# Optimization experiments

Measured on AMD Instinct MI355X. Metric: run time of the kernel, lower is better.

## Reference

```python
import jax, jax.numpy as jnp
import numpy as np

T, B, D, H = 512, 256, 256, 512


def setup_inputs() -> dict:
    key = jax.random.key(0)
    k1, k2, k3, k4 = jax.random.split(key, 4)
    x = jax.random.normal(k1, (T, B, D), dtype=jnp.float32)
    hidden_state = jnp.zeros((1, B, H), dtype=jnp.float32)
    episode_starts = jax.random.randint(k2, (T, B), 0, 2, dtype=jnp.int32)
    # PyTorch GRU params, gate order (r, z, n); xavier-ish / orthogonal-ish scale via randn*scale
    w_ih = jax.random.normal(k3, (3 * H, D), dtype=jnp.float32) * (1.0 / np.sqrt(D))
    w_hh = jax.random.normal(k4, (3 * H, H), dtype=jnp.float32) * (1.0 / np.sqrt(H))
    b_ih = jnp.zeros((3 * H,), dtype=jnp.float32)
    b_hh = jnp.zeros((3 * H,), dtype=jnp.float32)
    return {"x": x, "hidden_state": hidden_state, "episode_starts": episode_starts,
            "w_ih": w_ih, "w_hh": w_hh, "b_ih": b_ih, "b_hh": b_hh}


def _gru_scan(x, h0, episode_starts, w_ih, w_hh, b_ih, b_hh):
    # Precompute input projections for all timesteps: [T, B, 3H]
    gi_all = jnp.einsum('tbd,gd->tbg', x, w_ih) + b_ih
    keep_all = 1.0 - (episode_starts != 0).astype(x.dtype)  # [T, B]
    hsz = h0.shape[-1]

    def step(h, inputs):
        gi, keep = inputs          # gi: [B, 3H], keep: [B]
        h = h * keep[:, None]      # episode reset
        gh = h @ w_hh.T + b_hh     # [B, 3H]
        gi_r, gi_z, gi_n = gi[:, :hsz], gi[:, hsz:2 * hsz], gi[:, 2 * hsz:]
        gh_r, gh_z, gh_n = gh[:, :hsz], gh[:, hsz:2 * hsz], gh[:, 2 * hsz:]
        r = jax.nn.sigmoid(gi_r + gh_r)
        z = jax.nn.sigmoid(gi_z + gh_z)
        n = jnp.tanh(gi_n + r * gh_n)
        h_new = (1.0 - z) * n + z * h
        return h_new, h_new

    h_final, outputs = jax.lax.scan(step, h0, (gi_all, keep_all))
    return outputs, h_final


def reference(x, hidden_state, episode_starts, w_ih, w_hh, b_ih, b_hh):
    h0 = hidden_state[0]  # num_layers=1 -> [B, H]
    outputs, h_final = _gru_scan(x, h0, episode_starts, w_ih, w_hh, b_ih, b_hh)
    return outputs, h_final[None]  # ([T, B, H], [1, B, H])
```

## Files before the change

### kernel.cpp

```cpp
#include <hip/hip_runtime.h>
#include <stdint.h>

#define TT 512
#define BB 256
#define DD 256
#define HH 512

#define WSL 32
#define NGROUP 16
#define KS_X 8
#define KS_H 16
#define KS_TOT 24
#define NBLK 144

typedef __attribute__((ext_vector_type(8))) short short8;
typedef __attribute__((ext_vector_type(4))) float floatx4;
typedef __attribute__((ext_vector_type(4))) unsigned int uintx4;

__device__ __forceinline__ short f2bf(float v) {
    union { float f; uint32_t u; } x; x.f = v;
    uint32_t r = (x.u + 0x7fffu + ((x.u >> 16) & 1u)) >> 16;
    return (short)r;
}
__device__ __forceinline__ float bf2f_hi(unsigned int s) {
    union { uint32_t u; float f; } x; x.u = s & 0xffff0000u;
    return x.f;
}
__device__ __forceinline__ float sigm(float v) { return 1.0f / (1.0f + __expf(-v)); }

__global__ __launch_bounds__(256)
void clear_exch(unsigned int* e) {
    uintx4 v = {0xFFFFFFFFu, 0xFFFFFFFFu, 0xFFFFFFFFu, 0xFFFFFFFFu};
    *(uintx4*)(e + ((size_t)blockIdx.x * 256 + threadIdx.x) * 4) = v;
}

__global__ __launch_bounds__(128, 1)
void gru_persistent(const float* __restrict__ x,
                    const float* __restrict__ h0,
                    const int*   __restrict__ ep,
                    const float* __restrict__ w_ih,
                    const float* __restrict__ w_hh,
                    const float* __restrict__ b_ih,
                    const float* __restrict__ b_hh,
                    float* __restrict__ out,
                    unsigned int* __restrict__ exch) {
    __shared__ short ldsw[NBLK * 512];

    const int tid  = threadIdx.x;
    const int lane = tid & 63;
    const int w    = tid >> 6;
    const int b    = blockIdx.x;
    const int xcd = b & 7;
    const int idx = b >> 3;
    const int bg  = xcd * 2 + (idx >> 4);
    const int sl  = idx & 15;

    for (int u = tid; u < NBLK * 64; u += 128) {
        int blk = u >> 6;
        int l   = u & 63;
        int ww  = blk / 72;
        int rem = blk % 72;
        int g   = rem / 24;
        int ks  = rem % 24;
        int row = sl * WSL + ww * 16 + (l & 15) + g * HH;
        int k0  = ks * 32 + ((l >> 4) * 8);
        const float* src = (k0 < DD) ? (w_ih + (size_t)row * DD + k0)
                                     : (w_hh + (size_t)row * HH + (k0 - DD));
        short8 v;
        #pragma unroll
        for (int j = 0; j < 8; j++) v[j] = f2bf(src[j]);
        *(short8*)&ldsw[(size_t)blk * 512 + l * 8] = v;
    }
    __syncthreads();

    const int cl   = lane & 15;
    const int col  = sl * WSL + w * 16 + cl;
    const int am   = bg * 16 + cl;
    const int rbase = (lane >> 4) * 4;
    const int k0a  = (lane >> 4) * 8;
    const float br0 = b_ih[col] + b_hh[col];
    const float bz0 = b_ih[col + HH] + b_hh[col + HH];
    const float bin = b_ih[col + 2 * HH];
    const float bhn = b_hh[col + 2 * HH];

    for (int t = 0; t < TT; t++) {
        floatx4 accI[3], accH[3];
        #pragma unroll
        for (int g = 0; g < 3; g++) {
            accI[g] = (floatx4){0.f, 0.f, 0.f, 0.f};
            accH[g] = (floatx4){0.f, 0.f, 0.f, 0.f};
        }

        const float* xrow = x + ((size_t)t * BB + am) * DD;
        #pragma unroll
        for (int ks = 0; ks < KS_X; ks++) {
            int k0 = ks * 32 + k0a;
            short8 a;
            #pragma unroll
            for (int j = 0; j < 8; j++) a[j] = f2bf(xrow[k0 + j]);
            #pragma unroll
            for (int g = 0; g < 3; g++) {
                short8 bf = *(const short8*)&ldsw[(size_t)((w * 3 + g) * KS_TOT + ks) * 512 + lane * 8];
                accI[g] = __builtin_amdgcn_mfma_f32_16x16x32_bf16(a, bf, accI[g], 0, 0, 0);
            }
        }
        const float keepA = (ep[t * BB + am] != 0) ? 0.0f : 1.0f;

        short8 a[KS_H];
        float hprev_raw[4];
        if (t == 0) {
            const float* hrow = h0 + (size_t)am * HH;
            #pragma unroll
            for (int ks = 0; ks < KS_H; ks++) {
                int k0 = ks * 32 + k0a;
                #pragma unroll
                for (int j = 0; j < 8; j++) a[ks][j] = f2bf(hrow[k0 + j] * keepA);
            }
            #pragma unroll
            for (int j = 0; j < 4; j++)
                hprev_raw[j] = h0[(size_t)(bg * 16 + rbase + j) * HH + col];
        } else {
            const unsigned int tgt = (unsigned int)(t - 1);
            const unsigned int* exr = exch + ((size_t)((t & 1) ^ 1)) * BB * HH;
            const unsigned int* hb  = exr + (size_t)am * HH + k0a;
            const unsigned int* hq0 = exr + (size_t)(bg * 16 + rbase) * HH + col;
            const unsigned int* hq2 = exr + (size_t)(bg * 16 + rbase + 2) * HH + col;
            uintx4 u0[KS_H], u1[KS_H];
            unsigned int hp[4];
            for (;;) {
                #pragma unroll
                for (int ks = 0; ks < KS_H; ks++) {
                    asm volatile("global_load_dwordx4 %0, %2, off offset:%c3 sc0 sc1\n\t"
                                 "global_load_dwordx4 %1, %2, off offset:%c4 sc0 sc1"
                                 : "=&v"(u0[ks]), "=&v"(u1[ks])
                                 : "v"(hb), "n"(ks * 128), "n"(ks * 128 + 16)
                                 : "memory");
                }
                asm volatile("global_load_dword %0, %2, off sc0 sc1\n\t"
                             "global_load_dword %1, %2, off offset:2048 sc0 sc1"
                             : "=&v"(hp[0]), "=&v"(hp[1]) : "v"(hq0) : "memory");
                asm volatile("global_load_dword %0, %2, off sc0 sc1\n\t"
                             "global_load_dword %1, %2, off offset:2048 sc0 sc1"
                             : "=&v"(hp[2]), "=&v"(hp[3]) : "v"(hq2) : "memory");
                asm volatile("s_waitcnt vmcnt(0)" ::: "memory");
                __builtin_amdgcn_sched_barrier(0);
                unsigned int bad = 0;
                #pragma unroll
                for (int ks = 0; ks < KS_H; ks++) {
                    #pragma unroll
                    for (int j = 0; j < 4; j++) {
                        bad |= (u0[ks][j] ^ tgt) & 0xffffu;
                        bad |= (u1[ks][j] ^ tgt) & 0xffffu;
                    }
                }
                #pragma unroll
                for (int j = 0; j < 4; j++) bad |= (hp[j] ^ tgt) & 0xffffu;
                if (__all(bad == 0)) break;
                __builtin_amdgcn_s_sleep(1);
            }
            #pragma unroll
            for (int ks = 0; ks < KS_H; ks++) {
                union { short8 s; uintx4 u; } cv;
                cv.u[0] = (u0[ks][1] & 0xffff0000u) | (u0[ks][0] >> 16);
                cv.u[1] = (u0[ks][3] & 0xffff0000u) | (u0[ks][2] >> 16);
                cv.u[2] = (u1[ks][1] & 0xffff0000u) | (u1[ks][0] >> 16);
                cv.u[3] = (u1[ks][3] & 0xffff0000u) | (u1[ks][2] >> 16);
                a[ks] = cv.s;
            }
            if (keepA == 0.0f) {
                #pragma unroll
                for (int ks = 0; ks < KS_H; ks++) a[ks] = (short8)0;
            }
            #pragma unroll
            for (int j = 0; j < 4; j++) hprev_raw[j] = bf2f_hi(hp[j]);
        }

        #pragma unroll
        for (int ks = 0; ks < KS_H; ks++) {
            #pragma unroll
            for (int g = 0; g < 3; g++) {
                short8 bf = *(const short8*)&ldsw[(size_t)((w * 3 + g) * KS_TOT + KS_X + ks) * 512 + lane * 8];
                accH[g] = __builtin_amdgcn_mfma_f32_16x16x32_bf16(a[ks], bf, accH[g], 0, 0, 0);
            }
        }

        unsigned int* exw = exch + ((size_t)(t & 1)) * BB * HH;
        float hnv[4];
        #pragma unroll
        for (int j = 0; j < 4; j++) {
            const int mo = bg * 16 + rbase + j;
            const float keep = (ep[t * BB + mo] != 0) ? 0.0f : 1.0f;
            const float hprev = hprev_raw[j] * keep;
            const float r = sigm(accI[0][j] + accH[0][j] + br0);
            const float z = sigm(accI[1][j] + accH[1][j] + bz0);
            const float n = tanhf(accI[2][j] + bin + r * (accH[2][j] + bhn));
            hnv[j] = (1.0f - z) * n + z * hprev;
            if (t < TT - 1) {
                unsigned int* pw = exw + (size_t)mo * HH + col;
                unsigned int word = (((unsigned int)(unsigned short)f2bf(hnv[j])) << 16)
                                  | (unsigned int)(t & 0xffff);
                asm volatile("global_store_dword %0, %1, off sc0 sc1"
                             :: "v"(pw), "v"(word) : "memory");
            }
        }

        #pragma unroll
        for (int j = 0; j < 4; j++) {
            const int mo = bg * 16 + rbase + j;
            out[((size_t)t * BB + mo) * HH + col] = hnv[j];
            if (t == TT - 1) out[(size_t)TT * BB * HH + (size_t)mo * HH + col] = hnv[j];
        }
    }
}

extern "C" void kernel_launch(void* const* d_in, const int* in_sizes, int n_in,
                              void* d_out, int out_size, void* d_ws, size_t ws_size,
                              hipStream_t stream) {
    const float* x   = (const float*)d_in[0];
    const float* h0  = (const float*)d_in[1];
    const int*   ep  = (const int*)d_in[2];
    const float* wih = (const float*)d_in[3];
    const float* whh = (const float*)d_in[4];
    const float* bih = (const float*)d_in[5];
    const float* bhh = (const float*)d_in[6];
    float* out = (float*)d_out;

    unsigned int* exch = (unsigned int*)d_ws;

    hipLaunchKernelGGL(clear_exch, dim3(256), dim3(256), 0, stream, exch);
    hipLaunchKernelGGL(gru_persistent, dim3(256), dim3(128), 0, stream,
                       x, h0, ep, wih, whh, bih, bhh, out, exch);
}
```

Before: 3.299 ms.

## Exchange hidden state through per-XCD L2 with a system-coherent mirror fallback

```diff
diff --git a/kernel.cpp b/kernel.cpp
--- a/kernel.cpp
+++ b/kernel.cpp
@@ -12,6 +12,8 @@
 #define KS_H 16
 #define KS_TOT 24
 #define NBLK 144
+#define TAG_OFF 7
+#define FAST_TRIES 40
 
 typedef __attribute__((ext_vector_type(8))) short short8;
 typedef __attribute__((ext_vector_type(4))) float floatx4;
@@ -28,10 +30,11 @@
 }
 __device__ __forceinline__ float sigm(float v) { return 1.0f / (1.0f + __expf(-v)); }
 
-__global__ __launch_bounds__(256)
-void clear_exch(unsigned int* e) {
-    uintx4 v = {0xFFFFFFFFu, 0xFFFFFFFFu, 0xFFFFFFFFu, 0xFFFFFFFFu};
-    *(uintx4*)(e + ((size_t)blockIdx.x * 256 + threadIdx.x) * 4) = v;
+__global__ __launch_bounds__(64)
+void clear_ws(unsigned int* xcnt) {
+    if (threadIdx.x < 8)
+        __hip_atomic_store(&xcnt[threadIdx.x], 0u, __ATOMIC_RELAXED,
+                           __HIP_MEMORY_SCOPE_AGENT);
 }
 
 __global__ __launch_bounds__(128, 1)
@@ -43,17 +46,27 @@
                     const float* __restrict__ b_ih,
                     const float* __restrict__ b_hh,
                     float* __restrict__ out,
-                    unsigned int* __restrict__ exch) {
+                    unsigned int* __restrict__ fx,
+                    unsigned int* __restrict__ mx,
+                    unsigned int* __restrict__ xcnt) {
     __shared__ short ldsw[NBLK * 512];
+    __shared__ int s_rank;
 
     const int tid  = threadIdx.x;
     const int lane = tid & 63;
     const int w    = tid >> 6;
-    const int b    = blockIdx.x;
-    const int xcd = b & 7;
-    const int idx = b >> 3;
-    const int bg  = xcd * 2 + (idx >> 4);
-    const int sl  = idx & 15;
+
+    if (tid == 0) {
+        unsigned int xcc;
+        asm volatile("s_getreg_b32 %0, hwreg(HW_REG_XCC_ID)" : "=s"(xcc));
+        unsigned int r = __hip_atomic_fetch_add(&xcnt[xcc & 7], 1u,
+                                                __ATOMIC_RELAXED, __HIP_MEMORY_SCOPE_AGENT);
+        s_rank = (int)(((xcc & 7) * 32 + r) & 255);
+    }
+    __syncthreads();
+    const int rk = s_rank;
+    const int bg = rk >> 4;
+    const int sl = rk & 15;
 
     for (int u = tid; u < NBLK * 64; u += 128) {
         int blk = u >> 6;
@@ -95,13 +108,18 @@
         #pragma unroll
         for (int ks = 0; ks < KS_X; ks++) {
             int k0 = ks * 32 + k0a;
-            short8 a;
-            #pragma unroll
-            for (int j = 0; j < 8; j++) a[j] = f2bf(xrow[k0 + j]);
+            floatx4 f0 = *(const floatx4*)(xrow + k0);
+            floatx4 f1 = *(const floatx4*)(xrow + k0 + 4);
+            union { uintx4 u; short8 s; } cv;
+            asm("v_cvt_pk_bf16_f32 %0, %1, %2" : "=v"(cv.u[0]) : "v"(f0[0]), "v"(f0[1]));
+            asm("v_cvt_pk_bf16_f32 %0, %1, %2" : "=v"(cv.u[1]) : "v"(f0[2]), "v"(f0[3]));
+            asm("v_cvt_pk_bf16_f32 %0, %1, %2" : "=v"(cv.u[2]) : "v"(f1[0]), "v"(f1[1]));
+            asm("v_cvt_pk_bf16_f32 %0, %1, %2" : "=v"(cv.u[3]) : "v"(f1[2]), "v"(f1[3]));
+            const short8 av = cv.s;
             #pragma unroll
             for (int g = 0; g < 3; g++) {
                 short8 bf = *(const short8*)&ldsw[(size_t)((w * 3 + g) * KS_TOT + ks) * 512 + lane * 8];
-                accI[g] = __builtin_amdgcn_mfma_f32_16x16x32_bf16(a, bf, accI[g], 0, 0, 0);
+                accI[g] = __builtin_amdgcn_mfma_f32_16x16x32_bf16(av, bf, accI[g], 0, 0, 0);
             }
         }
         const float keepA = (ep[t * BB + am] != 0) ? 0.0f : 1.0f;
@@ -120,28 +138,33 @@
             for (int j = 0; j < 4; j++)
                 hprev_raw[j] = h0[(size_t)(bg * 16 + rbase + j) * HH + col];
         } else {
-            const unsigned int tgt = (unsigned int)(t - 1);
-            const unsigned int* exr = exch + ((size_t)((t & 1) ^ 1)) * BB * HH;
-            const unsigned int* hb  = exr + (size_t)am * HH + k0a;
-            const unsigned int* hq0 = exr + (size_t)(bg * 16 + rbase) * HH + col;
-            const unsigned int* hq2 = exr + (size_t)(bg * 16 + rbase + 2) * HH + col;
+            const unsigned int tgt = (unsigned int)(t - 1 + TAG_OFF);
+            const size_t roff = ((size_t)((t & 1) ^ 1)) * BB * HH;
+            const unsigned int* fb  = fx + roff + (size_t)am * HH + k0a;
+            const unsigned int* fq0 = fx + roff + (size_t)(bg * 16 + rbase) * HH + col;
+            const unsigned int* fq2 = fx + roff + (size_t)(bg * 16 + rbase + 2) * HH + col;
+            const unsigned int* mb  = mx + roff + (size_t)am * HH + k0a;
+            const unsigned int* mq0 = mx + roff + (size_t)(bg * 16 + rbase) * HH + col;
+            const unsigned int* mq2 = mx + roff + (size_t)(bg * 16 + rbase + 2) * HH + col;
             uintx4 u0[KS_H], u1[KS_H];
             unsigned int hp[4];
+            bool need_mirror = false;
+            int tries = 0;
             for (;;) {
                 #pragma unroll
                 for (int ks = 0; ks < KS_H; ks++) {
-                    asm volatile("global_load_dwordx4 %0, %2, off offset:%c3 sc0 sc1\n\t"
-                                 "global_load_dwordx4 %1, %2, off offset:%c4 sc0 sc1"
+                    asm volatile("global_load_dwordx4 %0, %2, off offset:%c3 sc0\n\t"
+                                 "global_load_dwordx4 %1, %2, off offset:%c4 sc0"
                                  : "=&v"(u0[ks]), "=&v"(u1[ks])
-                                 : "v"(hb), "n"(ks * 128), "n"(ks * 128 + 16)
+                                 : "v"(fb), "n"(ks * 128), "n"(ks * 128 + 16)
                                  : "memory");
                 }
-                asm volatile("global_load_dword %0, %2, off sc0 sc1\n\t"
-                             "global_load_dword %1, %2, off offset:2048 sc0 sc1"
-                             : "=&v"(hp[0]), "=&v"(hp[1]) : "v"(hq0) : "memory");
-                asm volatile("global_load_dword %0, %2, off sc0 sc1\n\t"
-                             "global_load_dword %1, %2, off offset:2048 sc0 sc1"
-                             : "=&v"(hp[2]), "=&v"(hp[3]) : "v"(hq2) : "memory");
+                asm volatile("global_load_dword %0, %2, off sc0\n\t"
+                             "global_load_dword %1, %2, off offset:2048 sc0"
+                             : "=&v"(hp[0]), "=&v"(hp[1]) : "v"(fq0) : "memory");
+                asm volatile("global_load_dword %0, %2, off sc0\n\t"
+                             "global_load_dword %1, %2, off offset:2048 sc0"
+                             : "=&v"(hp[2]), "=&v"(hp[3]) : "v"(fq2) : "memory");
                 asm volatile("s_waitcnt vmcnt(0)" ::: "memory");
                 __builtin_amdgcn_sched_barrier(0);
                 unsigned int bad = 0;
@@ -156,7 +179,41 @@
                 #pragma unroll
                 for (int j = 0; j < 4; j++) bad |= (hp[j] ^ tgt) & 0xffffu;
                 if (__all(bad == 0)) break;
+                if (++tries >= FAST_TRIES) { need_mirror = true; break; }
                 __builtin_amdgcn_s_sleep(1);
+            }
+            if (need_mirror) {
+                for (;;) {
+                    #pragma unroll
+                    for (int ks = 0; ks < KS_H; ks++) {
+                        asm volatile("global_load_dwordx4 %0, %2, off offset:%c3 sc0 sc1\n\t"
+                                     "global_load_dwordx4 %1, %2, off offset:%c4 sc0 sc1"
+                                     : "=&v"(u0[ks]), "=&v"(u1[ks])
+                                     : "v"(mb), "n"(ks * 128), "n"(ks * 128 + 16)
+                                     : "memory");
+                    }
+                    asm volatile("global_load_dword %0, %2, off sc0 sc1\n\t"
+                                 "global_load_dword %1, %2, off offset:2048 sc0 sc1"
+                                 : "=&v"(hp[0]), "=&v"(hp[1]) : "v"(mq0) : "memory");
+                    asm volatile("global_load_dword %0, %2, off sc0 sc1\n\t"
+                                 "global_load_dword %1, %2, off offset:2048 sc0 sc1"
+                                 : "=&v"(hp[2]), "=&v"(hp[3]) : "v"(mq2) : "memory");
+                    asm volatile("s_waitcnt vmcnt(0)" ::: "memory");
+                    __builtin_amdgcn_sched_barrier(0);
+                    unsigned int bad = 0;
+                    #pragma unroll
+                    for (int ks = 0; ks < KS_H; ks++) {
+                        #pragma unroll
+                        for (int j = 0; j < 4; j++) {
+                            bad |= (u0[ks][j] ^ tgt) & 0xffffu;
+                            bad |= (u1[ks][j] ^ tgt) & 0xffffu;
+                        }
+                    }
+                    #pragma unroll
+                    for (int j = 0; j < 4; j++) bad |= (hp[j] ^ tgt) & 0xffffu;
+                    if (__all(bad == 0)) break;
+                    __builtin_amdgcn_s_sleep(2);
+                }
             }
             #pragma unroll
             for (int ks = 0; ks < KS_H; ks++) {
@@ -184,7 +241,7 @@
             }
         }
 
-        unsigned int* exw = exch + ((size_t)(t & 1)) * BB * HH;
+        const size_t woff = ((size_t)(t & 1)) * BB * HH;
         float hnv[4];
         #pragma unroll
         for (int j = 0; j < 4; j++) {
@@ -196,11 +253,14 @@
             const float n = tanhf(accI[2][j] + bin + r * (accH[2][j] + bhn));
             hnv[j] = (1.0f - z) * n + z * hprev;
             if (t < TT - 1) {
-                unsigned int* pw = exw + (size_t)mo * HH + col;
                 unsigned int word = (((unsigned int)(unsigned short)f2bf(hnv[j])) << 16)
-                                  | (unsigned int)(t & 0xffff);
+                                  | (unsigned int)((t + TAG_OFF) & 0xffff);
+                unsigned int* pf = fx + woff + (size_t)mo * HH + col;
+                unsigned int* pm = mx + woff + (size_t)mo * HH + col;
+                asm volatile("global_store_dword %0, %1, off"
+                             :: "v"(pf), "v"(word) : "memory");
                 asm volatile("global_store_dword %0, %1, off sc0 sc1"
-                             :: "v"(pw), "v"(word) : "memory");
+                             :: "v"(pm), "v"(word) : "memory");
             }
         }
 
@@ -225,9 +285,11 @@
     const float* bhh = (const float*)d_in[6];
     float* out = (float*)d_out;
 
-    unsigned int* exch = (unsigned int*)d_ws;
-
-    hipLaunchKernelGGL(clear_exch, dim3(256), dim3(256), 0, stream, exch);
+    unsigned int* fx   = (unsigned int*)d_ws;
+    unsigned int* mx   = (unsigned int*)((char*)d_ws + 1048576);
+    unsigned int* xcnt = (unsigned int*)((char*)d_ws + 2097152);
+
+    hipLaunchKernelGGL(clear_ws, dim3(1), dim3(64), 0, stream, xcnt);
     hipLaunchKernelGGL(gru_persistent, dim3(256), dim3(128), 0, stream,
-                       x, h0, ep, wih, whh, bih, bhh, out, exch);
-}
+                       x, h0, ep, wih, whh, bih, bhh, out, fx, mx, xcnt);
+}
```

Result: slower. 4.085 ms (+23.8%).
